# Kernel tuning notes

Hardware: AMD Instinct MI355X
Metric: run time of the kernel (lower is better)

## Reference

```python
import jax, jax.numpy as jnp
import numpy as np
from functools import partial

# dims
BATCH, L, H = 1, 512, 2048
NH, HD = 64, 64            # num heads, head dim
INTER = NH * HD            # 4096
G, N = 4, 64               # n_groups, ssm state size
K = 4                      # conv kernel
CONV = INTER + 2 * G * N   # 4608
PROJ = INTER + CONV + NH   # z, xBC, dt
EPS = 1e-5


def rmsnorm(x, w, eps=EPS):
    xf = x.astype(jnp.float32)
    v = jnp.mean(xf * xf, axis=-1, keepdims=True)
    return (xf * jax.lax.rsqrt(v + eps)).astype(x.dtype) * w


def setup_inputs() -> dict:
    key = jax.random.key(0)
    ks = jax.random.split(key, 12)
    rn = lambda k, s, sc=1.0: sc * jax.random.normal(k, s, dtype=jnp.float32)
    return {
        "hidden_states": rn(ks[0], (BATCH, L, H)),
        "residual": rn(ks[1], (BATCH, L, H)),
        "norm_w": 1.0 + rn(ks[2], (H,), 0.02),
        "in_proj_w": rn(ks[3], (H, PROJ), 0.02),
        "conv_w": rn(ks[4], (CONV, K), 0.2),
        "conv_b": rn(ks[5], (CONV,), 0.02),
        "A_log": jnp.log(jax.random.uniform(ks[6], (NH,), minval=1.0, maxval=16.0)),
        "dt_bias": rn(ks[7], (NH,), 0.5),
        "D": rn(ks[8], (NH,), 0.5),
        "gn_w": 1.0 + rn(ks[9], (INTER,), 0.02),
        "out_proj_w": rn(ks[10], (INTER, H), 0.02),
    }


def reference(hidden_states, residual, norm_w, in_proj_w, conv_w, conv_b,
              A_log, dt_bias, D, gn_w, out_proj_w):
    B_ = hidden_states.shape[0]
    # fused add + RMSNorm (residual is not None path)
    x = hidden_states + residual
    new_residual = x
    hs = rmsnorm(x, norm_w)

    # in_proj: [B,L,H] -> [B,L,PROJ] split into z | xBC | dt
    proj = jnp.einsum('blh,hp->blp', hs, in_proj_w)
    z = proj[..., :INTER]
    xBC = proj[..., INTER:INTER + CONV]
    dt = proj[..., INTER + CONV:]

    # causal depthwise conv of width K, then SiLU
    xp = jnp.pad(xBC, ((0, 0), (K - 1, 0), (0, 0)))
    conv = sum(xp[:, k:k + L, :] * conv_w[None, None, :, k] for k in range(K))
    xBC = jax.nn.silu(conv + conv_b)

    xh = xBC[..., :INTER].reshape(B_, L, NH, HD)
    Bm = xBC[..., INTER:INTER + G * N].reshape(B_, L, G, N)
    Cm = xBC[..., INTER + G * N:].reshape(B_, L, G, N)

    dt = jax.nn.softplus(dt + dt_bias)          # [B,L,NH]
    A = -jnp.exp(A_log)                         # [NH]
    dA = jnp.exp(dt * A)                        # [B,L,NH]

    hpg = NH // G
    Bh = jnp.repeat(Bm, hpg, axis=2)            # [B,L,NH,N]
    Ch = jnp.repeat(Cm, hpg, axis=2)

    def step(h, inp):
        dA_t, dt_t, x_t, B_t, C_t = inp
        # h: [B,NH,HD,N]
        h = h * dA_t[:, :, None, None] + (dt_t[:, :, None] * x_t)[..., None] * B_t[:, :, None, :]
        y = jnp.einsum('bhdn,bhn->bhd', h, C_t)
        return h, y

    h0 = jnp.zeros((B_, NH, HD, N), dtype=jnp.float32)
    xs = (jnp.moveaxis(dA, 1, 0), jnp.moveaxis(dt, 1, 0), jnp.moveaxis(xh, 1, 0),
          jnp.moveaxis(Bh, 1, 0), jnp.moveaxis(Ch, 1, 0))
    _, ys = jax.lax.scan(step, h0, xs)          # [L,B,NH,HD]
    y = jnp.moveaxis(ys, 0, 1) + xh * D[None, None, :, None]
    y = y.reshape(B_, L, INTER)

    # gated RMSNorm then out_proj
    y = rmsnorm(y * jax.nn.silu(z), gn_w)
    out = jnp.einsum('bli,ih->blh', y, out_proj_w)
    return out, new_residual
```

## Files before the change

kernel.cpp:

```cpp
#include <hip/hip_runtime.h>
#include <stdint.h>

#define LSEQ 512
#define HDIM 2048
#define NH 64
#define HD 64
#define INTER 4096
#define NG 4
#define NSTATE 64
#define CONVC 4608
#define PROJC 8768
#define EPS 1e-5f
#define CL 64
#define NC 8
#define NHDN (NH * HD * NSTATE)

typedef __attribute__((ext_vector_type(8))) short bf16x8;
typedef __attribute__((ext_vector_type(4))) short short4v;
typedef __attribute__((ext_vector_type(4))) float f32x4;

__device__ __forceinline__ short f2bf(float f) {
  union { float f; uint32_t u; } v; v.f = f;
  uint32_t r = v.u + 0x7FFFu + ((v.u >> 16) & 1u);
  return (short)(r >> 16);
}

__device__ __forceinline__ uint32_t cvt_pk_bf16(float lo, float hi) {
  uint32_t r;
  asm("v_cvt_pk_bf16_f32 %0, %1, %2" : "=v"(r) : "v"(lo), "v"(hi));
  return r;
}

__device__ __forceinline__ float bf2f(short s) {
  union { uint32_t u; float f; } v; v.u = ((uint32_t)(uint16_t)s) << 16;
  return v.f;
}

__device__ __forceinline__ float siluf(float v) {
  return v / (1.f + expf(-v));
}

__device__ __forceinline__ int xcd_swizzle(int orig, int nwg) {
  int q = nwg >> 3, r = nwg & 7;
  int xcd = orig & 7, idx = orig >> 3;
  return (xcd < r ? xcd * (q + 1) : r * (q + 1) + (xcd - r) * q) + idx;
}

__global__ __launch_bounds__(256) void k_add_rmsnorm(
    const float* __restrict__ hid, const float* __restrict__ res,
    const float* __restrict__ w, float* __restrict__ resid_out,
    short* __restrict__ hsb) {
  __shared__ float sred[4];
  const int row = blockIdx.x, tid = threadIdx.x;
  const float4* h4 = (const float4*)(hid + (size_t)row * HDIM);
  const float4* r4 = (const float4*)(res + (size_t)row * HDIM);
  float4* ro4 = (float4*)(resid_out + (size_t)row * HDIM);
  float4 a0 = h4[tid], b0 = r4[tid];
  float4 a1 = h4[tid + 256], b1 = r4[tid + 256];
  float4 xa, xb;
  xa.x = a0.x + b0.x; xa.y = a0.y + b0.y; xa.z = a0.z + b0.z; xa.w = a0.w + b0.w;
  xb.x = a1.x + b1.x; xb.y = a1.y + b1.y; xb.z = a1.z + b1.z; xb.w = a1.w + b1.w;
  ro4[tid] = xa; ro4[tid + 256] = xb;
  float ss = xa.x*xa.x + xa.y*xa.y + xa.z*xa.z + xa.w*xa.w
           + xb.x*xb.x + xb.y*xb.y + xb.z*xb.z + xb.w*xb.w;
  #pragma unroll
  for (int off = 32; off >= 1; off >>= 1) ss += __shfl_down(ss, off);
  if ((tid & 63) == 0) sred[tid >> 6] = ss;
  __syncthreads();
  float tot = sred[0] + sred[1] + sred[2] + sred[3];
  float rs = rsqrtf(tot / (float)HDIM + EPS);
  int e0 = tid * 4, e1 = (tid + 256) * 4;
  short4v s0, s1;
  s0.x = f2bf(xa.x * rs * w[e0+0]); s0.y = f2bf(xa.y * rs * w[e0+1]);
  s0.z = f2bf(xa.z * rs * w[e0+2]); s0.w = f2bf(xa.w * rs * w[e0+3]);
  s1.x = f2bf(xb.x * rs * w[e1+0]); s1.y = f2bf(xb.y * rs * w[e1+1]);
  s1.z = f2bf(xb.z * rs * w[e1+2]); s1.w = f2bf(xb.w * rs * w[e1+3]);
  *(short4v*)(hsb + (size_t)row * HDIM + e0) = s0;
  *(short4v*)(hsb + (size_t)row * HDIM + e1) = s1;
}

__global__ __launch_bounds__(256) void k_transpose_cvt(
    const float* __restrict__ src, short* __restrict__ dst, int R, int C) {
  __shared__ float tile[32][33];
  const int tx = threadIdx.x & 31, ty = threadIdx.x >> 5;
  const int c0 = blockIdx.x * 32, r0 = blockIdx.y * 32;
  #pragma unroll
  for (int i = 0; i < 4; ++i)
    tile[ty + i*8][tx] = src[(size_t)(r0 + ty + i*8) * C + c0 + tx];
  __syncthreads();
  #pragma unroll
  for (int i = 0; i < 4; ++i)
    dst[(size_t)(c0 + ty + i*8) * R + r0 + tx] = f2bf(tile[tx][ty + i*8]);
}

__global__ __launch_bounds__(256) void k_gemm1(
    const short* __restrict__ A, const float* __restrict__ Bw,
    short* __restrict__ zbf, short* __restrict__ xbc,
    float* __restrict__ dtf) {
  constexpr int BM = 128, MR = 4, WROWS = 64;
  const int M = LSEQ, N = PROJC, K = HDIM;
  __shared__ short lA[2][BM * 64];
  __shared__ short lB[2][64 * 64];
  const int tid = threadIdx.x, lane = tid & 63, wid = tid >> 6;

  const int NMB = M / BM, NNB = N / 64;
  const int nwg = NMB * NNB;
  int wg = xcd_swizzle(blockIdx.x, nwg);
  const int mi = wg % NMB;
  const int ni = wg / NMB;
  const int m0 = mi * BM, n0 = ni * 64;
  const int wm = wid >> 1, wn = wid & 1;

  const int lrow8 = lane >> 3;
  const int cswz = ((lane & 7) ^ lrow8) * 8;

  auto stageA = [&](int buf, int kt) {
    #pragma unroll
    for (int r2 = 0; r2 < MR; ++r2) {
      int idx = r2 * 4 + wid;
      __builtin_amdgcn_global_load_lds(
          (const __attribute__((address_space(1))) int*)(A + (size_t)(m0 + idx * 8 + lrow8) * K + kt + cswz),
          (__attribute__((address_space(3))) int*)(&lA[buf][idx * 512]),
          16, 0, 0);
    }
  };

  float breg[16];
  auto loadB = [&](int kt) {
    #pragma unroll
    for (int r = 0; r < 2; ++r)
      #pragma unroll
      for (int j = 0; j < 8; ++j)
        breg[r * 8 + j] = Bw[(size_t)(kt + wid * 16 + r * 8 + j) * N + n0 + lane];
  };
  auto writeB = [&](int buf) {
    #pragma unroll
    for (int r = 0; r < 2; ++r) {
      uint4 v;
      v.x = cvt_pk_bf16(breg[r*8+0], breg[r*8+1]);
      v.y = cvt_pk_bf16(breg[r*8+2], breg[r*8+3]);
      v.z = cvt_pk_bf16(breg[r*8+4], breg[r*8+5]);
      v.w = cvt_pk_bf16(breg[r*8+6], breg[r*8+7]);
      int ko = wid * 2 + r;
      *(uint4*)&lB[buf][lane * 64 + ((ko ^ (lane & 7)) << 3)] = v;
    }
  };

  f32x4 acc[MR][2] = {};
  const int lrow = lane & 15, lkb = (lane >> 4) * 8;
  const int NT = K >> 6;
  loadB(0);
  stageA(0, 0);
  writeB(0);
  asm volatile("s_waitcnt vmcnt(0)" ::: "memory");
  __builtin_amdgcn_s_barrier();
  for (int t = 0; t < NT; ++t) {
    int cur = t & 1;
    if (t + 1 < NT) {
      loadB((t + 1) * 64);
      stageA(cur ^ 1, (t + 1) * 64);
    }
    #pragma unroll
    for (int kk = 0; kk < 2; ++kk) {
      bf16x8 a[MR], b[2];
      #pragma unroll
      for (int m = 0; m < MR; ++m) {
        int row = wm * WROWS + m * 16 + lrow;
        int colel = (kk * 32 + lkb) ^ ((row & 7) << 3);
        a[m] = *(const bf16x8*)&lA[cur][row * 64 + colel];
      }
      #pragma unroll
      for (int n = 0; n < 2; ++n) {
        int row = wn * 32 + n * 16 + lrow;
        int colel = (kk * 32 + lkb) ^ ((row & 7) << 3);
        b[n] = *(const bf16x8*)&lB[cur][row * 64 + colel];
      }
      #pragma unroll
      for (int m = 0; m < MR; ++m)
        #pragma unroll
        for (int n = 0; n < 2; ++n)
          acc[m][n] = __builtin_amdgcn_mfma_f32_16x16x32_bf16(a[m], b[n], acc[m][n], 0, 0, 0);
    }
    if (t + 1 < NT) writeB(cur ^ 1);
    asm volatile("s_waitcnt vmcnt(0)" ::: "memory");
    __builtin_amdgcn_s_barrier();
  }
  #pragma unroll
  for (int m = 0; m < MR; ++m) {
    int row = m0 + wm * WROWS + m * 16 + (lane >> 4) * 4;
    #pragma unroll
    for (int n = 0; n < 2; ++n) {
      int coll = wn * 32 + n * 16 + (lane & 15);
      #pragma unroll
      for (int r = 0; r < 4; ++r) {
        float v = acc[m][n][r];
        if (ni < 64)
          zbf[(size_t)(row + r) * INTER + n0 + coll] = f2bf(v);
        else if (ni < 136)
          xbc[(size_t)(row + r) * CONVC + (n0 - INTER) + coll] = f2bf(v);
        else
          dtf[(row + r) * 64 + coll] = v;
      }
    }
  }
}

template <int BM, int KS>
__global__ __launch_bounds__(256) void k_gemm_bf16(
    const short* __restrict__ A, const short* __restrict__ B,
    float* __restrict__ C, int M, int N, int K) {
  __shared__ short lA[2][BM * 64];
  __shared__ short lB[2][64 * 64];
  const int tid = threadIdx.x;
  const int lane = tid & 63, wid = tid >> 6;
  constexpr int MR = BM / 32;
  constexpr int WROWS = BM / 2;

  const int NMB = M / BM, NNB = N / 64;
  const int nwg = NMB * NNB * KS;
  int wg = xcd_swizzle(blockIdx.x, nwg);
  const int mi = wg % NMB;
  int rest = wg / NMB;
  const int zi = (KS > 1) ? (rest % KS) : 0;
  const int ni = (KS > 1) ? (rest / KS) : rest;
  const int m0 = mi * BM, n0 = ni * 64;
  const int wm = wid >> 1, wn = wid & 1;

  const int lrow8 = lane >> 3;
  const int cswz = ((lane & 7) ^ lrow8) * 8;

  const int Kc = K / KS;
  const int kbase = zi * Kc;
  float* Cp = C + (size_t)zi * M * N;

  auto stage = [&](int buf, int kt) {
    #pragma unroll
    for (int r2 = 0; r2 < MR; ++r2) {
      int idx = r2 * 4 + wid;
      __builtin_amdgcn_global_load_lds(
          (const __attribute__((address_space(1))) int*)(A + (size_t)(m0 + idx * 8 + lrow8) * K + kt + cswz),
          (__attribute__((address_space(3))) int*)(&lA[buf][idx * 512]),
          16, 0, 0);
    }
    #pragma unroll
    for (int r2 = 0; r2 < 2; ++r2) {
      int idx = r2 * 4 + wid;
      __builtin_amdgcn_global_load_lds(
          (const __attribute__((address_space(1))) int*)(B + (size_t)(n0 + idx * 8 + lrow8) * K + kt + cswz),
          (__attribute__((address_space(3))) int*)(&lB[buf][idx * 512]),
          16, 0, 0);
    }
  };

  f32x4 acc[MR][2] = {};
  const int lrow = lane & 15, lkb = (lane >> 4) * 8;
  const int NT = Kc >> 6;
  stage(0, kbase);
  for (int t = 0; t < NT; ++t) {
    int cur = t & 1;
    if (t + 1 < NT) {
      stage(cur ^ 1, kbase + (t + 1) * 64);
      if constexpr (MR == 2) asm volatile("s_waitcnt vmcnt(4)" ::: "memory");
      else                   asm volatile("s_waitcnt vmcnt(6)" ::: "memory");
    } else {
      asm volatile("s_waitcnt vmcnt(0)" ::: "memory");
    }
    __builtin_amdgcn_s_barrier();
    #pragma unroll
    for (int kk = 0; kk < 2; ++kk) {
      bf16x8 a[MR], b[2];
      #pragma unroll
      for (int m = 0; m < MR; ++m) {
        int row = wm * WROWS + m * 16 + lrow;
        int colel = (kk * 32 + lkb) ^ ((row & 7) << 3);
        a[m] = *(const bf16x8*)&lA[cur][row * 64 + colel];
      }
      #pragma unroll
      for (int n = 0; n < 2; ++n) {
        int row = wn * 32 + n * 16 + lrow;
        int colel = (kk * 32 + lkb) ^ ((row & 7) << 3);
        b[n] = *(const bf16x8*)&lB[cur][row * 64 + colel];
      }
      #pragma unroll
      for (int m = 0; m < MR; ++m)
        #pragma unroll
        for (int n = 0; n < 2; ++n)
          acc[m][n] = __builtin_amdgcn_mfma_f32_16x16x32_bf16(a[m], b[n], acc[m][n], 0, 0, 0);
    }
    __builtin_amdgcn_s_barrier();
  }
  #pragma unroll
  for (int m = 0; m < MR; ++m) {
    int row = m0 + wm * WROWS + m * 16 + (lane >> 4) * 4;
    int col = n0 + wn * 32 + (lane & 15);
    #pragma unroll
    for (int n = 0; n < 2; ++n)
      #pragma unroll
      for (int r = 0; r < 4; ++r)
        Cp[(size_t)(row + r) * N + col + n * 16] = acc[m][n][r];
  }
}

__global__ __launch_bounds__(256) void k_reduce2(
    const float* __restrict__ p, float* __restrict__ out, int n) {
  int i = (blockIdx.x * 256 + threadIdx.x) * 4;
  float4 a = *(const float4*)(p + i);
  float4 b = *(const float4*)(p + n + i);
  float4 o;
  o.x = a.x + b.x; o.y = a.y + b.y; o.z = a.z + b.z; o.w = a.w + b.w;
  *(float4*)(out + i) = o;
}

__global__ __launch_bounds__(256) void k_conv(
    const short* __restrict__ xbc, const float* __restrict__ dtf,
    const float* __restrict__ cw, const float* __restrict__ cb,
    const float* __restrict__ A_log, const float* __restrict__ dt_bias,
    short* __restrict__ convo, float* __restrict__ dtb,
    float* __restrict__ ldab) {
  const int l0 = blockIdx.y * 64;
  if (blockIdx.x == CONVC / 256) {
    #pragma unroll
    for (int i = 0; i < 16; ++i) {
      int idx = threadIdx.x + i * 256;
      int l = l0 + (idx >> 6), h = idx & 63;
      float v = dtf[l * 64 + h] + dt_bias[h];
      float dt = v > 20.f ? v : log1pf(expf(v));
      float lda = dt * (-expf(A_log[h]));
      dtb[h * LSEQ + l] = dt;
      ldab[h * LSEQ + l] = lda;
    }
    return;
  }
  const int c = blockIdx.x * 256 + threadIdx.x;
  const float w0 = cw[c*4+0], w1 = cw[c*4+1], w2 = cw[c*4+2], w3 = cw[c*4+3];
  const float bias = cb[c];
  float x0 = 0.f, x1 = 0.f, x2 = 0.f;
  if (l0 > 0) {
    x0 = bf2f(xbc[(size_t)(l0-3) * CONVC + c]);
    x1 = bf2f(xbc[(size_t)(l0-2) * CONVC + c]);
    x2 = bf2f(xbc[(size_t)(l0-1) * CONVC + c]);
  }
  for (int l = l0; l < l0 + 64; ++l) {
    float x3 = bf2f(xbc[(size_t)l * CONVC + c]);
    float accv = bias + x0*w0 + x1*w1 + x2*w2 + x3*w3;
    convo[(size_t)l * CONVC + c] = f2bf(siluf(accv));
    x0 = x1; x1 = x2; x2 = x3;
  }
}

__global__ __launch_bounds__(256) void k_ssd(
    const short* __restrict__ convo, const float* __restrict__ dtb,
    const float* __restrict__ ldab, const float* __restrict__ Dp,
    float* __restrict__ ybuf, float* __restrict__ hend,
    float* __restrict__ Pbuf, float* __restrict__ cdbuf) {
  __shared__ __align__(16) short Xt[64 * 72];
  __shared__ __align__(16) short Bs[64 * 72];
  __shared__ __align__(16) short Cs[64 * 72];
  __shared__ __align__(16) short Btw[64 * 72];
  __shared__ __align__(16) short Ms[64 * 72];
  __shared__ float s_s[64], s_dt[64], s_w[64];
  const int c = blockIdx.x, head = blockIdx.y;
  const int g = head >> 4;
  const int tid = threadIdx.x, lane = tid & 63, wid = tid >> 6;
  const int l0 = c * CL;
  const short* xbase = convo + (size_t)l0 * CONVC + head * HD;
  const short* Bbase = convo + (size_t)l0 * CONVC + INTER + g * NSTATE;
  const short* Cbase = convo + (size_t)l0 * CONVC + INTER + NG * NSTATE + g * NSTATE;

  if (tid < 64) {
    float ps = ldab[head * LSEQ + l0 + tid];
    #pragma unroll
    for (int o = 1; o < 64; o <<= 1) {
      float u = __shfl_up(ps, o);
      if (tid >= o) ps += u;
    }
    float dtv = dtb[head * LSEQ + l0 + tid];
    s_s[tid] = ps;
    s_dt[tid] = dtv;
    float s63 = __shfl(ps, 63);
    s_w[tid] = __expf(s63 - ps) * dtv;
    cdbuf[head * LSEQ + l0 + tid] = __expf(ps);
    if (tid == 63) Pbuf[c * NH + head] = __expf(ps);
  }
  #pragma unroll
  for (int rep = 0; rep < 4; ++rep) {
    int l = (tid >> 4) + rep * 16;
    int d = (tid & 15) * 4;
    size_t roff = (size_t)l * CONVC;
    short4v xv = *(const short4v*)(xbase + roff + d);
    Xt[(d + 0) * 72 + l] = xv.x;
    Xt[(d + 1) * 72 + l] = xv.y;
    Xt[(d + 2) * 72 + l] = xv.z;
    Xt[(d + 3) * 72 + l] = xv.w;
    *(short4v*)&Bs[l * 72 + d] = *(const short4v*)(Bbase + roff + d);
    *(short4v*)&Cs[l * 72 + d] = *(const short4v*)(Cbase + roff + d);
  }
  __syncthreads();
  #pragma unroll
  for (int rep = 0; rep < 16; ++rep) {
    int idx = rep * 256 + tid;
    int l = idx >> 6, n = idx & 63;
    Btw[n * 72 + l] = f2bf(bf2f(Bs[l * 72 + n]) * s_w[l]);
  }
  __syncthreads();
  const int lrow = lane & 15, lkb = (lane >> 4) * 8;
  f32x4 sacc[4] = {};
  f32x4 hacc[4] = {};
  #pragma unroll
  for (int kk = 0; kk < 2; ++kk) {
    bf16x8 ac = *(const bf16x8*)&Cs[(wid * 16 + lrow) * 72 + kk * 32 + lkb];
    bf16x8 ax = *(const bf16x8*)&Xt[(wid * 16 + lrow) * 72 + kk * 32 + lkb];
    #pragma unroll
    for (int t4 = 0; t4 < 4; ++t4) {
      bf16x8 bb = *(const bf16x8*)&Bs[(t4 * 16 + lrow) * 72 + kk * 32 + lkb];
      bf16x8 bw = *(const bf16x8*)&Btw[(t4 * 16 + lrow) * 72 + kk * 32 + lkb];
      sacc[t4] = __builtin_amdgcn_mfma_f32_16x16x32_bf16(ac, bb, sacc[t4], 0, 0, 0);
      hacc[t4] = __builtin_amdgcn_mfma_f32_16x16x32_bf16(ax, bw, hacc[t4], 0, 0, 0);
    }
  }
  float* hb = hend + ((size_t)c * NH + head) * (HD * NSTATE);
  #pragma unroll
  for (int t4 = 0; t4 < 4; ++t4) {
    int j = t4 * 16 + lrow;
    float sj = s_s[j], dtj = s_dt[j];
    #pragma unroll
    for (int r = 0; r < 4; ++r) {
      int i = wid * 16 + (lane >> 4) * 4 + r;
      float m = (j <= i) ? __expf(s_s[i] - sj) * dtj * sacc[t4][r] : 0.f;
      Ms[i * 72 + j] = f2bf(m);
      hb[i * NSTATE + j] = hacc[t4][r];
    }
  }
  __syncthreads();
  f32x4 yacc[4] = {};
  #pragma unroll
  for (int kk = 0; kk < 2; ++kk) {
    bf16x8 am = *(const bf16x8*)&Ms[(wid * 16 + lrow) * 72 + kk * 32 + lkb];
    #pragma unroll
    for (int t4 = 0; t4 < 4; ++t4) {
      bf16x8 bx = *(const bf16x8*)&Xt[(t4 * 16 + lrow) * 72 + kk * 32 + lkb];
      yacc[t4] = __builtin_amdgcn_mfma_f32_16x16x32_bf16(am, bx, yacc[t4], 0, 0, 0);
    }
  }
  const float Dv = Dp[head];
  #pragma unroll
  for (int t4 = 0; t4 < 4; ++t4) {
    int d = t4 * 16 + lrow;
    #pragma unroll
    for (int r = 0; r < 4; ++r) {
      int i = wid * 16 + (lane >> 4) * 4 + r;
      float xv = bf2f(Xt[d * 72 + i]);
      ybuf[(size_t)(l0 + i) * INTER + head * HD + d] = yacc[t4][r] + xv * Dv;
    }
  }
}

__global__ __launch_bounds__(256) void k_scan_combine(
    const float* __restrict__ hend, const float* __restrict__ Pbuf,
    float* __restrict__ hinbuf) {
  const int e = blockIdx.x * 256 + threadIdx.x;
  const int head = e >> 12;
  float h = 0.f;
  #pragma unroll
  for (int c = 1; c < NC; ++c) {
    h = Pbuf[(c - 1) * NH + head] * h + hend[(size_t)(c - 1) * NHDN + e];
    hinbuf[(size_t)c * NHDN + e] = h;
  }
}

__global__ __launch_bounds__(256) void k_scan_fixup(
    const short* __restrict__ convo, const float* __restrict__ hinbuf,
    const float* __restrict__ cdbuf, float* __restrict__ ybuf) {
  __shared__ float sh[NSTATE][HD + 1];
  __shared__ float sc[CL][NSTATE];
  __shared__ float scd[CL];
  const int bid = blockIdx.x;
  const int c = (bid >> 6) + 1, head = bid & 63, g = head >> 4;
  const int t = threadIdx.x;
  #pragma unroll
  for (int i = 0; i < 16; ++i) {
    int idx = t + i * 256;
    int d = idx >> 6, n = idx & 63;
    sh[n][d] = hinbuf[(size_t)c * NHDN + head * (HD * NSTATE) + idx];
  }
  #pragma unroll
  for (int i = 0; i < 16; ++i) {
    int idx = t + i * 256;
    int ll = idx >> 6, n = idx & 63;
    sc[ll][n] = bf2f(convo[(size_t)(c * CL + ll) * CONVC + INTER + NG * NSTATE + g * NSTATE + n]);
  }
  if (t < CL) scd[t] = cdbuf[head * LSEQ + c * CL + t];
  __syncthreads();
  const int d = t & 63, w = t >> 6;
  #pragma unroll
  for (int i = 0; i < 4; ++i) {
    int l0 = i * 16 + w * 4;
    float a0 = 0.f, a1 = 0.f, a2 = 0.f, a3 = 0.f;
    for (int n = 0; n < NSTATE; ++n) {
      float hv = sh[n][d];
      a0 += hv * sc[l0 + 0][n];
      a1 += hv * sc[l0 + 1][n];
      a2 += hv * sc[l0 + 2][n];
      a3 += hv * sc[l0 + 3][n];
    }
    size_t base = (size_t)(c * CL + l0) * INTER + head * HD + d;
    ybuf[base + 0 * INTER] += scd[l0 + 0] * a0;
    ybuf[base + 1 * INTER] += scd[l0 + 1] * a1;
    ybuf[base + 2 * INTER] += scd[l0 + 2] * a2;
    ybuf[base + 3 * INTER] += scd[l0 + 3] * a3;
  }
}

__global__ __launch_bounds__(256) void k_gated_norm(
    const float* __restrict__ ybuf, const short* __restrict__ zbf,
    const float* __restrict__ gw, short* __restrict__ y2b) {
  __shared__ float sred[4];
  const int row = blockIdx.x, tid = threadIdx.x;
  const float4* y4 = (const float4*)(ybuf + (size_t)row * INTER);
  const short4v* z4 = (const short4v*)(zbf + (size_t)row * INTER);
  float g[16];
  float ss = 0.f;
  #pragma unroll
  for (int i = 0; i < 4; ++i) {
    float4 y = y4[tid + i * 256];
    short4v z = z4[tid + i * 256];
    float g0 = y.x * siluf(bf2f(z.x)), g1 = y.y * siluf(bf2f(z.y));
    float g2 = y.z * siluf(bf2f(z.z)), g3 = y.w * siluf(bf2f(z.w));
    g[i*4+0] = g0; g[i*4+1] = g1; g[i*4+2] = g2; g[i*4+3] = g3;
    ss += g0*g0 + g1*g1 + g2*g2 + g3*g3;
  }
  #pragma unroll
  for (int off = 32; off >= 1; off >>= 1) ss += __shfl_down(ss, off);
  if ((tid & 63) == 0) sred[tid >> 6] = ss;
  __syncthreads();
  float tot = sred[0] + sred[1] + sred[2] + sred[3];
  float rs = rsqrtf(tot / (float)INTER + EPS);
  #pragma unroll
  for (int i = 0; i < 4; ++i) {
    int e = (tid + i * 256) * 4;
    short4v s;
    s.x = f2bf(g[i*4+0] * rs * gw[e+0]);
    s.y = f2bf(g[i*4+1] * rs * gw[e+1]);
    s.z = f2bf(g[i*4+2] * rs * gw[e+2]);
    s.w = f2bf(g[i*4+3] * rs * gw[e+3]);
    *(short4v*)(y2b + (size_t)row * INTER + e) = s;
  }
}

extern "C" void kernel_launch(void* const* d_in, const int* in_sizes, int n_in,
                              void* d_out, int out_size, void* d_ws, size_t ws_size,
                              hipStream_t stream) {
  const float* hid     = (const float*)d_in[0];
  const float* res     = (const float*)d_in[1];
  const float* norm_w  = (const float*)d_in[2];
  const float* w1      = (const float*)d_in[3];
  const float* cw      = (const float*)d_in[4];
  const float* cb      = (const float*)d_in[5];
  const float* A_log   = (const float*)d_in[6];
  const float* dt_bias = (const float*)d_in[7];
  const float* Dp      = (const float*)d_in[8];
  const float* gw      = (const float*)d_in[9];
  const float* w2      = (const float*)d_in[10];

  float* out = (float*)d_out;
  float* resid_out = out + (size_t)LSEQ * HDIM;

  char* ws = (char*)d_ws;
  short* hsb  = (short*)(ws);
  float* hend   = (float*)(ws + 2097152);
  float* p2     = (float*)(ws + 2097152);
  float* hinbuf = (float*)(ws + 10485760);
  float* Pbuf   = (float*)(ws + 18874368);
  float* cdbuf  = (float*)(ws + 18876416);
  short* zbf  = (short*)(ws + 38010880);
  short* xbc  = (short*)(ws + 42205184);
  float* dtf  = (float*)(ws + 46923776);
  short* convo= (short*)(ws + 55967744);
  float* dtb  = (float*)(ws + 65404928);
  float* ldab = (float*)(ws + 65536000);
  float* ybuf = (float*)(ws + 65667072);
  short* y2b  = (short*)(ws + 74055680);
  short* w2t  = (short*)(ws + 78249984);

  k_add_rmsnorm<<<LSEQ, 256, 0, stream>>>(hid, res, norm_w, resid_out, hsb);
  k_gemm1<<<(LSEQ/128)*(PROJC/64), 256, 0, stream>>>(hsb, w1, zbf, xbc, dtf);
  k_conv<<<dim3(CONVC/256 + 1, NC), 256, 0, stream>>>(xbc, dtf, cw, cb, A_log, dt_bias, convo, dtb, ldab);
  k_ssd<<<dim3(NC, NH), 256, 0, stream>>>(convo, dtb, ldab, Dp, ybuf, hend, Pbuf, cdbuf);
  k_scan_combine<<<NHDN/256, 256, 0, stream>>>(hend, Pbuf, hinbuf);
  k_scan_fixup<<<(NC-1)*NH, 256, 0, stream>>>(convo, hinbuf, cdbuf, ybuf);
  k_gated_norm<<<LSEQ, 256, 0, stream>>>(ybuf, zbf, gw, y2b);
  k_transpose_cvt<<<dim3(HDIM/32, INTER/32), 256, 0, stream>>>(w2, w2t, INTER, HDIM);
  k_gemm_bf16<64, 2><<<(LSEQ/64)*(HDIM/64)*2, 256, 0, stream>>>(y2b, w2t, p2, LSEQ, HDIM, INTER);
  k_reduce2<<<LSEQ*HDIM/1024, 256, 0, stream>>>(p2, out, LSEQ*HDIM);
}
```

Before: 135.9 us.

## Single-buffer B tile in gemm1, store y in bf16, use split-K 4 for out_proj

The in_proj GEMM now keeps one LDS buffer for the B tile instead of two and adds an extra barrier before each write, which lowers LDS use but serialises the B write behind the compute. The SSD output buffer ybuf is stored as bf16 instead of fp32, halving its traffic through the ssd, fixup and gated-norm kernels at some cost in precision. The out_proj GEMM moves from split-K 2 to split-K 4 for more parallelism, and the reduction kernel now sums four partials. The p2 partials region must be large enough to hold four slices.

```diff
diff --git a/kernel.cpp b/kernel.cpp
--- a/kernel.cpp
+++ b/kernel.cpp
@@ -100,7 +100,7 @@
   constexpr int BM = 128, MR = 4, WROWS = 64;
   const int M = LSEQ, N = PROJC, K = HDIM;
   __shared__ short lA[2][BM * 64];
-  __shared__ short lB[2][64 * 64];
+  __shared__ short lB[64 * 64];
   const int tid = threadIdx.x, lane = tid & 63, wid = tid >> 6;
 
   const int NMB = M / BM, NNB = N / 64;
@@ -133,7 +133,7 @@
       for (int j = 0; j < 8; ++j)
         breg[r * 8 + j] = Bw[(size_t)(kt + wid * 16 + r * 8 + j) * N + n0 + lane];
   };
-  auto writeB = [&](int buf) {
+  auto writeB = [&]() {
     #pragma unroll
     for (int r = 0; r < 2; ++r) {
       uint4 v;
@@ -142,7 +142,7 @@
       v.z = cvt_pk_bf16(breg[r*8+4], breg[r*8+5]);
       v.w = cvt_pk_bf16(breg[r*8+6], breg[r*8+7]);
       int ko = wid * 2 + r;
-      *(uint4*)&lB[buf][lane * 64 + ((ko ^ (lane & 7)) << 3)] = v;
+      *(uint4*)&lB[lane * 64 + ((ko ^ (lane & 7)) << 3)] = v;
     }
   };
 
@@ -151,8 +151,9 @@
   const int NT = K >> 6;
   loadB(0);
   stageA(0, 0);
-  writeB(0);
+  writeB();
   asm volatile("s_waitcnt vmcnt(0)" ::: "memory");
+  asm volatile("s_waitcnt lgkmcnt(0)" ::: "memory");
   __builtin_amdgcn_s_barrier();
   for (int t = 0; t < NT; ++t) {
     int cur = t & 1;
@@ -173,7 +174,7 @@
       for (int n = 0; n < 2; ++n) {
         int row = wn * 32 + n * 16 + lrow;
         int colel = (kk * 32 + lkb) ^ ((row & 7) << 3);
-        b[n] = *(const bf16x8*)&lB[cur][row * 64 + colel];
+        b[n] = *(const bf16x8*)&lB[row * 64 + colel];
       }
       #pragma unroll
       for (int m = 0; m < MR; ++m)
@@ -181,8 +182,10 @@
         for (int n = 0; n < 2; ++n)
           acc[m][n] = __builtin_amdgcn_mfma_f32_16x16x32_bf16(a[m], b[n], acc[m][n], 0, 0, 0);
     }
-    if (t + 1 < NT) writeB(cur ^ 1);
+    __builtin_amdgcn_s_barrier();
+    if (t + 1 < NT) writeB();
     asm volatile("s_waitcnt vmcnt(0)" ::: "memory");
+    asm volatile("s_waitcnt lgkmcnt(0)" ::: "memory");
     __builtin_amdgcn_s_barrier();
   }
   #pragma unroll
@@ -301,13 +304,18 @@
   }
 }
 
-__global__ __launch_bounds__(256) void k_reduce2(
+__global__ __launch_bounds__(256) void k_reduce4(
     const float* __restrict__ p, float* __restrict__ out, int n) {
   int i = (blockIdx.x * 256 + threadIdx.x) * 4;
   float4 a = *(const float4*)(p + i);
   float4 b = *(const float4*)(p + n + i);
+  float4 c = *(const float4*)(p + 2 * (size_t)n + i);
+  float4 d = *(const float4*)(p + 3 * (size_t)n + i);
   float4 o;
-  o.x = a.x + b.x; o.y = a.y + b.y; o.z = a.z + b.z; o.w = a.w + b.w;
+  o.x = (a.x + b.x) + (c.x + d.x);
+  o.y = (a.y + b.y) + (c.y + d.y);
+  o.z = (a.z + b.z) + (c.z + d.z);
+  o.w = (a.w + b.w) + (c.w + d.w);
   *(float4*)(out + i) = o;
 }
 
@@ -351,7 +359,7 @@
 __global__ __launch_bounds__(256) void k_ssd(
     const short* __restrict__ convo, const float* __restrict__ dtb,
     const float* __restrict__ ldab, const float* __restrict__ Dp,
-    float* __restrict__ ybuf, float* __restrict__ hend,
+    short* __restrict__ ybuf, float* __restrict__ hend,
     float* __restrict__ Pbuf, float* __restrict__ cdbuf) {
   __shared__ __align__(16) short Xt[64 * 72];
   __shared__ __align__(16) short Bs[64 * 72];
@@ -450,7 +458,7 @@
     for (int r = 0; r < 4; ++r) {
       int i = wid * 16 + (lane >> 4) * 4 + r;
       float xv = bf2f(Xt[d * 72 + i]);
-      ybuf[(size_t)(l0 + i) * INTER + head * HD + d] = yacc[t4][r] + xv * Dv;
+      ybuf[(size_t)(l0 + i) * INTER + head * HD + d] = f2bf(yacc[t4][r] + xv * Dv);
     }
   }
 }
@@ -470,7 +478,7 @@
 
 __global__ __launch_bounds__(256) void k_scan_fixup(
     const short* __restrict__ convo, const float* __restrict__ hinbuf,
-    const float* __restrict__ cdbuf, float* __restrict__ ybuf) {
+    const float* __restrict__ cdbuf, short* __restrict__ ybuf) {
   __shared__ float sh[NSTATE][HD + 1];
   __shared__ float sc[CL][NSTATE];
   __shared__ float scd[CL];
@@ -504,28 +512,28 @@
       a3 += hv * sc[l0 + 3][n];
     }
     size_t base = (size_t)(c * CL + l0) * INTER + head * HD + d;
-    ybuf[base + 0 * INTER] += scd[l0 + 0] * a0;
-    ybuf[base + 1 * INTER] += scd[l0 + 1] * a1;
-    ybuf[base + 2 * INTER] += scd[l0 + 2] * a2;
-    ybuf[base + 3 * INTER] += scd[l0 + 3] * a3;
+    ybuf[base + 0 * INTER] = f2bf(bf2f(ybuf[base + 0 * INTER]) + scd[l0 + 0] * a0);
+    ybuf[base + 1 * INTER] = f2bf(bf2f(ybuf[base + 1 * INTER]) + scd[l0 + 1] * a1);
+    ybuf[base + 2 * INTER] = f2bf(bf2f(ybuf[base + 2 * INTER]) + scd[l0 + 2] * a2);
+    ybuf[base + 3 * INTER] = f2bf(bf2f(ybuf[base + 3 * INTER]) + scd[l0 + 3] * a3);
   }
 }
 
 __global__ __launch_bounds__(256) void k_gated_norm(
-    const float* __restrict__ ybuf, const short* __restrict__ zbf,
+    const short* __restrict__ ybuf, const short* __restrict__ zbf,
     const float* __restrict__ gw, short* __restrict__ y2b) {
   __shared__ float sred[4];
   const int row = blockIdx.x, tid = threadIdx.x;
-  const float4* y4 = (const float4*)(ybuf + (size_t)row * INTER);
+  const short4v* y4 = (const short4v*)(ybuf + (size_t)row * INTER);
   const short4v* z4 = (const short4v*)(zbf + (size_t)row * INTER);
   float g[16];
   float ss = 0.f;
   #pragma unroll
   for (int i = 0; i < 4; ++i) {
-    float4 y = y4[tid + i * 256];
+    short4v y = y4[tid + i * 256];
     short4v z = z4[tid + i * 256];
-    float g0 = y.x * siluf(bf2f(z.x)), g1 = y.y * siluf(bf2f(z.y));
-    float g2 = y.z * siluf(bf2f(z.z)), g3 = y.w * siluf(bf2f(z.w));
+    float g0 = bf2f(y.x) * siluf(bf2f(z.x)), g1 = bf2f(y.y) * siluf(bf2f(z.y));
+    float g2 = bf2f(y.z) * siluf(bf2f(z.z)), g3 = bf2f(y.w) * siluf(bf2f(z.w));
     g[i*4+0] = g0; g[i*4+1] = g1; g[i*4+2] = g2; g[i*4+3] = g3;
     ss += g0*g0 + g1*g1 + g2*g2 + g3*g3;
   }
@@ -578,7 +586,7 @@
   short* convo= (short*)(ws + 55967744);
   float* dtb  = (float*)(ws + 65404928);
   float* ldab = (float*)(ws + 65536000);
-  float* ybuf = (float*)(ws + 65667072);
+  short* ybuf = (short*)(ws + 65667072);
   short* y2b  = (short*)(ws + 74055680);
   short* w2t  = (short*)(ws + 78249984);
 
@@ -590,6 +598,6 @@
   k_scan_fixup<<<(NC-1)*NH, 256, 0, stream>>>(convo, hinbuf, cdbuf, ybuf);
   k_gated_norm<<<LSEQ, 256, 0, stream>>>(ybuf, zbf, gw, y2b);
   k_transpose_cvt<<<dim3(HDIM/32, INTER/32), 256, 0, stream>>>(w2, w2t, INTER, HDIM);
-  k_gemm_bf16<64, 2><<<(LSEQ/64)*(HDIM/64)*2, 256, 0, stream>>>(y2b, w2t, p2, LSEQ, HDIM, INTER);
-  k_reduce2<<<LSEQ*HDIM/1024, 256, 0, stream>>>(p2, out, LSEQ*HDIM);
-}
+  k_gemm_bf16<64, 4><<<(LSEQ/64)*(HDIM/64)*4, 256, 0, stream>>>(y2b, w2t, p2, LSEQ, HDIM, INTER);
+  k_reduce4<<<LSEQ*HDIM/1024, 256, 0, stream>>>(p2, out, LSEQ*HDIM);
+}
```

New measurement: 130.1 us. 1.04x faster.
